# Optimization experiments

Hardware: AMD Instinct MI355X
Metric: run time of the kernel (lower is better)

The kernel has to match this reference:

```python
import jax, jax.numpy as jnp
import numpy as np

N_NODES = 50000
N_EDGES = 600000
DIM_H = 128
LN_EPS = 1e-5


def setup_inputs() -> dict:
    key = jax.random.key(0)
    ks = jax.random.split(key, 8)
    s = 1.0 / np.sqrt(DIM_H)
    return {
        "nodes": jax.random.normal(ks[0], (N_NODES, DIM_H), jnp.float32),
        "W_msg": jax.random.normal(ks[1], (DIM_H, DIM_H), jnp.float32) * s,
        "b_msg": jnp.zeros((DIM_H,), jnp.float32),
        "w_ih": jax.random.normal(ks[2], (3 * DIM_H, DIM_H), jnp.float32) * s,
        "w_hh": jax.random.normal(ks[3], (3 * DIM_H, DIM_H), jnp.float32) * s,
        "b_ih": jnp.zeros((3 * DIM_H,), jnp.float32),
        "b_hh": jnp.zeros((3 * DIM_H,), jnp.float32),
        "ln_gamma": jnp.ones((DIM_H,), jnp.float32),
        "ln_beta": jnp.zeros((DIM_H,), jnp.float32),
        "edge_src": jax.random.randint(ks[4], (N_EDGES,), 0, N_NODES, jnp.int32),
        "edge_dst": jax.random.randint(ks[5], (N_EDGES,), 0, N_NODES, jnp.int32),
    }


def _layer_norm(x, gamma, beta):
    mu = jnp.mean(x, axis=-1, keepdims=True)
    var = jnp.mean(jnp.square(x - mu), axis=-1, keepdims=True)
    return gamma * (x - mu) * jax.lax.rsqrt(var + LN_EPS) + beta


def reference(nodes, W_msg, b_msg, w_ih, w_hh, b_ih, b_hh, ln_gamma, ln_beta,
              edge_src, edge_dst):
    n_nodes = nodes.shape[0]
    # send_and_recv: per-edge message from source node, sum-reduce at dest
    msg_e = nodes[edge_src] @ W_msg.T + b_msg            # [E, H] (irregular gather)
    messages = jax.ops.segment_sum(msg_e, edge_dst, num_segments=n_nodes)  # [N, H]
    # global connection: add mean node feature
    msg = messages + jnp.mean(nodes, axis=0)
    # single-step GRU (torch gate layout: r, z, n)
    gi = msg @ w_ih.T + b_ih                             # [N, 3H]
    gh = nodes @ w_hh.T + b_hh                           # [N, 3H]
    i_r, i_z, i_n = jnp.split(gi, 3, axis=-1)
    h_r, h_z, h_n = jnp.split(gh, 3, axis=-1)
    r = jax.nn.sigmoid(i_r + h_r)
    z = jax.nn.sigmoid(i_z + h_z)
    n = jnp.tanh(i_n + r * h_n)
    h_next = (1.0 - z) * n + z * nodes
    # LayerNorm then post-GRU spatial residual with messages
    out = _layer_norm(h_next, ln_gamma, ln_beta)
    out = out + messages
    return out
```

## Files before the change

### kernel.cpp

```cpp
#include <hip/hip_runtime.h>
#include <hip/hip_bf16.h>

#define N_NODES 50000
#define N_EDGES 600000
#define DIM_H   128
#define NPAD    50048
#define NB_SCAN 196

typedef __attribute__((ext_vector_type(8))) short bf16x8;
typedef __attribute__((ext_vector_type(4))) float f32x4;
typedef __attribute__((ext_vector_type(4))) short short4v;

__device__ __forceinline__ short f2bs(float f) {
    __hip_bfloat16 h = __float2bfloat16(f);
    return *reinterpret_cast<short*>(&h);
}
__device__ __forceinline__ float bs2f(short s) {
    unsigned u = ((unsigned)(unsigned short)s) << 16;
    return __builtin_bit_cast(float, u);
}
__device__ __forceinline__ float sigm(float x) { return 1.f / (1.f + __expf(-x)); }
__device__ __forceinline__ float tanh_f(float x) {
    return 2.f / (1.f + __expf(-2.f * x)) - 1.f;
}
__device__ __forceinline__ unsigned pk2(float a, float b) {
    return ((unsigned)(unsigned short)f2bs(b) << 16) | (unsigned)(unsigned short)f2bs(a);
}
__device__ __forceinline__ float unlo(unsigned u) { return bs2f((short)(u & 0xffffu)); }
__device__ __forceinline__ float unhi(unsigned u) { return bs2f((short)(u >> 16)); }

__device__ __forceinline__ void dma16(const void* g, const void* lds_uniform) {
    __builtin_amdgcn_global_load_lds(
        (const __attribute__((address_space(1))) void*)g,
        (__attribute__((address_space(3))) void*)(unsigned)(unsigned long long)lds_uniform,
        16, 0, 0);
}

__global__ __launch_bounds__(256) void prep_k(const float* __restrict__ wmsg,
                                              const float* __restrict__ wih,
                                              const float* __restrict__ whh,
                                              short* __restrict__ wmsgB,
                                              short* __restrict__ wihB,
                                              short* __restrict__ whhB,
                                              int* __restrict__ cnt,
                                              float* __restrict__ colsum,
                                              short* __restrict__ aggTail,
                                              short* __restrict__ nodesTail) {
    int i = blockIdx.x * 256 + threadIdx.x;
    if (i < 16384) wmsgB[i] = f2bs(wmsg[i]);
    if (i < 49152) { wihB[i] = f2bs(wih[i]); whhB[i] = f2bs(whh[i]); }
    if (i < N_NODES) cnt[i] = 0;
    if (i < 128) colsum[i] = 0.f;
    if (i < 1536) {
        short4v z = {0, 0, 0, 0};
        *(short4v*)(aggTail   + i * 4) = z;
        *(short4v*)(nodesTail + i * 4) = z;
    }
}

__global__ __launch_bounds__(256) void colsum_k(const float* __restrict__ nodes,
                                                float* __restrict__ colsum,
                                                short* __restrict__ nodesB) {
    __shared__ float red[8][128];
    const int tid = threadIdx.x;
    const int cg = tid & 31;
    const int rl = tid >> 5;
    float4 acc = {0.f, 0.f, 0.f, 0.f};
    for (int r = blockIdx.x * 8 + rl; r < N_NODES; r += gridDim.x * 8) {
        float4 v = *(const float4*)(nodes + (size_t)r * DIM_H + cg * 4);
        acc.x += v.x; acc.y += v.y; acc.z += v.z; acc.w += v.w;
        *(short4v*)(nodesB + (size_t)r * DIM_H + cg * 4) =
            (short4v){f2bs(v.x), f2bs(v.y), f2bs(v.z), f2bs(v.w)};
    }
    *(float4*)&red[rl][cg * 4] = acc;
    __syncthreads();
    if (tid < 128) {
        float s = 0.f;
#pragma unroll
        for (int i = 0; i < 8; ++i) s += red[i][tid];
        unsafeAtomicAdd(&colsum[tid], s);
    }
}

__global__ __launch_bounds__(256) void hist_k(const int* __restrict__ edst,
                                              int* __restrict__ cnt) {
    int e = blockIdx.x * 256 + threadIdx.x;
    if (e < N_EDGES) atomicAdd(&cnt[edst[e]], 1);
}

__global__ __launch_bounds__(256) void bsum_k(const int* __restrict__ cnt,
                                              int* __restrict__ bsum) {
    const int t = threadIdx.x;
    int i = blockIdx.x * 256 + t;
    int v = (i < N_NODES) ? cnt[i] : 0;
#pragma unroll
    for (int o = 32; o; o >>= 1) v += __shfl_xor(v, o, 64);
    __shared__ int w4[4];
    if ((t & 63) == 0) w4[t >> 6] = v;
    __syncthreads();
    if (t == 0) bsum[blockIdx.x] = w4[0] + w4[1] + w4[2] + w4[3];
}

__global__ __launch_bounds__(256) void scan2_k(const int* __restrict__ cnt,
                                               const int* __restrict__ bsum,
                                               int* __restrict__ rowptr,
                                               int* __restrict__ pos) {
    const int b = blockIdx.x, t = threadIdx.x;
    const int lane = t & 63, w = t >> 6;
    __shared__ int red[4];
    __shared__ int wsum[4];

    int ov = (t < b) ? bsum[t] : 0;
#pragma unroll
    for (int o = 32; o; o >>= 1) ov += __shfl_xor(ov, o, 64);
    if (lane == 0) red[w] = ov;
    __syncthreads();
    const int offset = red[0] + red[1] + red[2] + red[3];

    int i = b * 256 + t;
    int v = (i < N_NODES) ? cnt[i] : 0;
    int x = v;
#pragma unroll
    for (int o = 1; o < 64; o <<= 1) {
        int y = __shfl_up(x, o, 64);
        if (lane >= o) x += y;
    }
    if (lane == 63) wsum[w] = x;
    __syncthreads();
    int woff = 0;
#pragma unroll
    for (int j = 0; j < 4; ++j)
        if (j < w) woff += wsum[j];
    int excl = offset + woff + (x - v);
    if (i < N_NODES) { rowptr[i] = excl; pos[i] = excl; }
    if (i == N_NODES - 1) rowptr[N_NODES] = excl + v;
}

__global__ __launch_bounds__(256) void reorder_k(const int* __restrict__ esrc,
                                                 const int* __restrict__ edst,
                                                 int* __restrict__ pos,
                                                 int* __restrict__ ssrc) {
    int e = blockIdx.x * 256 + threadIdx.x;
    if (e < N_EDGES) {
        int p = atomicAdd(&pos[edst[e]], 1);
        ssrc[p] = esrc[e];
    }
}

__global__ __launch_bounds__(256) void aggregate_k(const short* __restrict__ nodesB,
                                                   const int* __restrict__ rowptr,
                                                   const int* __restrict__ ssrc,
                                                   short* __restrict__ aggB) {
    const int wid = threadIdx.x >> 6;
    const int lane = threadIdx.x & 63;
    const int n = blockIdx.x * 4 + wid;
    if (n >= N_NODES) return;
    const int s0 = rowptr[n], s1 = rowptr[n + 1];
    float2 acc = {0.f, 0.f};
    int e = s0;
    for (; e + 3 < s1; e += 4) {
        int sa = ssrc[e], sb = ssrc[e + 1], sc = ssrc[e + 2], sd = ssrc[e + 3];
        short2 va = ((const short2*)(nodesB + (size_t)sa * DIM_H))[lane];
        short2 vb = ((const short2*)(nodesB + (size_t)sb * DIM_H))[lane];
        short2 vc = ((const short2*)(nodesB + (size_t)sc * DIM_H))[lane];
        short2 vd = ((const short2*)(nodesB + (size_t)sd * DIM_H))[lane];
        acc.x += (bs2f(va.x) + bs2f(vb.x)) + (bs2f(vc.x) + bs2f(vd.x));
        acc.y += (bs2f(va.y) + bs2f(vb.y)) + (bs2f(vc.y) + bs2f(vd.y));
    }
    for (; e < s1; ++e) {
        int sa = ssrc[e];
        short2 va = ((const short2*)(nodesB + (size_t)sa * DIM_H))[lane];
        acc.x += bs2f(va.x);
        acc.y += bs2f(va.y);
    }
    short2 o; o.x = f2bs(acc.x); o.y = f2bs(acc.y);
    ((short2*)(aggB + (size_t)n * DIM_H))[lane] = o;
}

template <int ROWS>
__device__ __forceinline__ void stage_tileT(const short* __restrict__ src, int row0,
                                            short* lds, int w, int lane) {
    constexpr int ITERS = ROWS / 16;
#pragma unroll
    for (int it = 0; it < ITERS; ++it) {
        int c = w * ITERS + it;
        int s = c * 64 + lane;
        int r = s >> 4, q = s & 15;
        int g = q ^ (r & 15);
        dma16(src + (((size_t)(row0 + r)) << 7) + (g << 3), lds + (size_t)c * 512);
    }
}

__device__ __forceinline__ void wave_mm64(const short* __restrict__ A,
                                          const short* __restrict__ W,
                                          f32x4 (&acc)[2][4],
                                          int wm, int wn, int r16, int half) {
#pragma unroll
    for (int kt = 0; kt < 4; ++kt) {
        const int kg = kt * 4 + half;
        const int sq = (kg ^ r16) << 3;
        bf16x8 af[2], bfr[4];
#pragma unroll
        for (int t = 0; t < 2; ++t)
            af[t] = *(const bf16x8*)&A[(wm + t * 16 + r16) * 128 + sq];
#pragma unroll
        for (int t = 0; t < 4; ++t)
            bfr[t] = *(const bf16x8*)&W[(wn + t * 16 + r16) * 128 + sq];
#pragma unroll
        for (int i = 0; i < 2; ++i)
#pragma unroll
            for (int j = 0; j < 4; ++j)
                acc[i][j] = __builtin_amdgcn_mfma_f32_16x16x32_bf16(
                    af[i], bfr[j], acc[i][j], 0, 0, 0);
    }
}

#define ZACC()                                        \
    _Pragma("unroll") for (int zi = 0; zi < 2; ++zi)  \
    _Pragma("unroll") for (int zj = 0; zj < 4; ++zj)  \
        acc[zi][zj] = (f32x4){0.f, 0.f, 0.f, 0.f}

__global__ __launch_bounds__(256) void fused_k(const short* __restrict__ aggB,
                                               const short* __restrict__ nodesB,
                                               const short* __restrict__ wmsgB,
                                               const short* __restrict__ wihB,
                                               const short* __restrict__ whhB,
                                               const float* __restrict__ bmsg,
                                               const float* __restrict__ bih,
                                               const float* __restrict__ bhh,
                                               const int* __restrict__ deg,
                                               const float* __restrict__ colsum,
                                               const float* __restrict__ gamma,
                                               const float* __restrict__ beta,
                                               float* __restrict__ out) {
    __shared__ short Ms[64 * 128];
    __shared__ short Ns[64 * 128];
    __shared__ short Wb[128 * 128];
    __shared__ float redS[64][2];
    __shared__ float redQ[64][2];

    const int tid = threadIdx.x;
    const int lane = tid & 63, w = tid >> 6;
    const int m0 = blockIdx.x * 64;
    const int r16 = lane & 15, half = lane >> 4;
    const int wm = (w >> 1) * 32, wn = (w & 1) * 64;
    const float invN = 1.0f / N_NODES;

    stage_tileT<64>(aggB, m0, Ms, w, lane);
    stage_tileT<64>(nodesB, m0, Ns, w, lane);
    stage_tileT<128>(wmsgB, 0, Wb, w, lane);
    __syncthreads();

    f32x4 acc[2][4];

    ZACC();
    wave_mm64(Ms, Wb, acc, wm, wn, r16, half);
    __syncthreads();
    stage_tileT<128>(wihB, 0, Wb, w, lane);
    {
        float bm[4], cs[4];
#pragma unroll
        for (int j = 0; j < 4; ++j) {
            int c = wn + j * 16 + r16;
            bm[j] = bmsg[c];
            cs[j] = colsum[c] * invN;
        }
#pragma unroll
        for (int i = 0; i < 2; ++i)
#pragma unroll
            for (int rr = 0; rr < 4; ++rr) {
                int lr = wm + i * 16 + half * 4 + rr;
                int gm = m0 + lr;
                float dg = (gm < N_NODES) ? (float)deg[gm] : 0.f;
#pragma unroll
                for (int j = 0; j < 4; ++j) {
                    int c = wn + j * 16 + r16;
                    float v = acc[i][j][rr] + dg * bm[j] + cs[j];
                    int slot = (c >> 3) ^ (lr & 15);
                    Ms[lr * 128 + slot * 8 + (c & 7)] = f2bs(v);
                }
            }
    }
    __syncthreads();

    ZACC();
    wave_mm64(Ms, Wb, acc, wm, wn, r16, half);
    __syncthreads();
    stage_tileT<128>(whhB, 0, Wb, w, lane);
    __syncthreads();
    wave_mm64(Ns, Wb, acc, wm, wn, r16, half);
    __syncthreads();
    stage_tileT<128>(wihB, 256, Wb, w, lane);
    unsigned rp[2][4][2];
    {
        float b0[4];
#pragma unroll
        for (int j = 0; j < 4; ++j) {
            int c = wn + j * 16 + r16;
            b0[j] = bih[c] + bhh[c];
        }
#pragma unroll
        for (int i = 0; i < 2; ++i)
#pragma unroll
            for (int j = 0; j < 4; ++j) {
                rp[i][j][0] = pk2(sigm(acc[i][j][0] + b0[j]), sigm(acc[i][j][1] + b0[j]));
                rp[i][j][1] = pk2(sigm(acc[i][j][2] + b0[j]), sigm(acc[i][j][3] + b0[j]));
            }
    }
    __syncthreads();

    ZACC();
    wave_mm64(Ms, Wb, acc, wm, wn, r16, half);
    __syncthreads();
    stage_tileT<128>(whhB, 256, Wb, w, lane);
    unsigned inp[2][4][2];
    {
        float bi[4];
#pragma unroll
        for (int j = 0; j < 4; ++j) bi[j] = bih[256 + wn + j * 16 + r16];
#pragma unroll
        for (int i = 0; i < 2; ++i)
#pragma unroll
            for (int j = 0; j < 4; ++j) {
                inp[i][j][0] = pk2(acc[i][j][0] + bi[j], acc[i][j][1] + bi[j]);
                inp[i][j][1] = pk2(acc[i][j][2] + bi[j], acc[i][j][3] + bi[j]);
            }
    }
    __syncthreads();

    ZACC();
    wave_mm64(Ns, Wb, acc, wm, wn, r16, half);
    __syncthreads();
    stage_tileT<128>(wihB, 128, Wb, w, lane);
    unsigned np_[2][4][2];
    {
        float bh[4];
#pragma unroll
        for (int j = 0; j < 4; ++j) bh[j] = bhh[256 + wn + j * 16 + r16];
#pragma unroll
        for (int i = 0; i < 2; ++i)
#pragma unroll
            for (int j = 0; j < 4; ++j) {
                float n0 = tanh_f(unlo(inp[i][j][0]) + unlo(rp[i][j][0]) * (acc[i][j][0] + bh[j]));
                float n1 = tanh_f(unhi(inp[i][j][0]) + unhi(rp[i][j][0]) * (acc[i][j][1] + bh[j]));
                float n2 = tanh_f(unlo(inp[i][j][1]) + unlo(rp[i][j][1]) * (acc[i][j][2] + bh[j]));
                float n3 = tanh_f(unhi(inp[i][j][1]) + unhi(rp[i][j][1]) * (acc[i][j][3] + bh[j]));
                np_[i][j][0] = pk2(n0, n1);
                np_[i][j][1] = pk2(n2, n3);
            }
    }
    __syncthreads();

    ZACC();
    wave_mm64(Ms, Wb, acc, wm, wn, r16, half);
    __syncthreads();
    stage_tileT<128>(whhB, 128, Wb, w, lane);
    __syncthreads();
    wave_mm64(Ns, Wb, acc, wm, wn, r16, half);
    {
        float b1[4];
#pragma unroll
        for (int j = 0; j < 4; ++j) {
            int c = wn + j * 16 + r16;
            b1[j] = bih[128 + c] + bhh[128 + c];
        }
#pragma unroll
        for (int i = 0; i < 2; ++i)
#pragma unroll
            for (int j = 0; j < 4; ++j)
#pragma unroll
                for (int rr = 0; rr < 4; ++rr) {
                    int lr = wm + i * 16 + half * 4 + rr;
                    int c = wn + j * 16 + r16;
                    int slot = (c >> 3) ^ (lr & 15);
                    float h = bs2f(Ns[lr * 128 + slot * 8 + (c & 7)]);
                    float z = sigm(acc[i][j][rr] + b1[j]);
                    float nv = (rr & 1) ? unhi(np_[i][j][rr >> 1]) : unlo(np_[i][j][rr >> 1]);
                    acc[i][j][rr] = (1.f - z) * nv + z * h;
                }
    }

#pragma unroll
    for (int i = 0; i < 2; ++i)
#pragma unroll
        for (int rr = 0; rr < 4; ++rr) {
            float s = acc[i][0][rr] + acc[i][1][rr] + acc[i][2][rr] + acc[i][3][rr];
            float q = acc[i][0][rr] * acc[i][0][rr] + acc[i][1][rr] * acc[i][1][rr]
                    + acc[i][2][rr] * acc[i][2][rr] + acc[i][3][rr] * acc[i][3][rr];
#pragma unroll
            for (int o = 1; o < 16; o <<= 1) {
                s += __shfl_xor(s, o, 64);
                q += __shfl_xor(q, o, 64);
            }
            if (r16 == 0) {
                int lr = wm + i * 16 + half * 4 + rr;
                redS[lr][wn >> 6] = s;
                redQ[lr][wn >> 6] = q;
            }
        }
    __syncthreads();

    {
        float ga[4], be[4], cs[4];
#pragma unroll
        for (int j = 0; j < 4; ++j) {
            int c = wn + j * 16 + r16;
            ga[j] = gamma[c];
            be[j] = beta[c];
            cs[j] = colsum[c] * invN;
        }
#pragma unroll
        for (int i = 0; i < 2; ++i)
#pragma unroll
            for (int rr = 0; rr < 4; ++rr) {
                int lr = wm + i * 16 + half * 4 + rr;
                int gm = m0 + lr;
                float S = redS[lr][0] + redS[lr][1];
                float Q = redQ[lr][0] + redQ[lr][1];
                float mu = S * (1.0f / DIM_H);
                float var = Q * (1.0f / DIM_H) - mu * mu;
                float rstd = rsqrtf(var + 1e-5f);
                if (gm < N_NODES) {
#pragma unroll
                    for (int j = 0; j < 4; ++j) {
                        int c = wn + j * 16 + r16;
                        int slot = (c >> 3) ^ (lr & 15);
                        float resid = bs2f(Ms[lr * 128 + slot * 8 + (c & 7)]) - cs[j];
                        out[(size_t)gm * DIM_H + c] =
                            ga[j] * (acc[i][j][rr] - mu) * rstd + be[j] + resid;
                    }
                }
            }
    }
}

extern "C" void kernel_launch(void* const* d_in, const int* in_sizes, int n_in,
                              void* d_out, int out_size, void* d_ws, size_t ws_size,
                              hipStream_t stream) {
    const float* nodes = (const float*)d_in[0];
    const float* Wmsg  = (const float*)d_in[1];
    const float* bmsg  = (const float*)d_in[2];
    const float* wih   = (const float*)d_in[3];
    const float* whh   = (const float*)d_in[4];
    const float* bih   = (const float*)d_in[5];
    const float* bhh   = (const float*)d_in[6];
    const float* gamma = (const float*)d_in[7];
    const float* beta  = (const float*)d_in[8];
    const int* esrc = (const int*)d_in[9];
    const int* edst = (const int*)d_in[10];
    float* out = (float*)d_out;

    char* ws = (char*)d_ws;
    short* aggB   = (short*)ws;
    short* nodesB = (short*)(ws + 12812288);
    short* wmsgB  = (short*)(ws + 25624576);
    short* wihB   = (short*)(ws + 25657344);
    short* whhB   = (short*)(ws + 25755648);
    float* colsum = (float*)(ws + 25853952);
    int*   cnt    = (int*)(ws + 25854464);
    int*   rowptr = (int*)(ws + 26054464);
    int*   pos    = (int*)(ws + 26254480);
    int*   ssrc   = (int*)(ws + 26454480);
    int*   bsum   = (int*)(ws + 28854480);

    short* aggTail   = aggB   + (size_t)N_NODES * DIM_H;
    short* nodesTail = nodesB + (size_t)N_NODES * DIM_H;

    prep_k<<<NB_SCAN, 256, 0, stream>>>(Wmsg, wih, whh, wmsgB, wihB, whhB,
                                        cnt, colsum, aggTail, nodesTail);
    colsum_k<<<512, 256, 0, stream>>>(nodes, colsum, nodesB);

    const int EB = (N_EDGES + 255) / 256;
    hist_k<<<EB, 256, 0, stream>>>(edst, cnt);
    bsum_k<<<NB_SCAN, 256, 0, stream>>>(cnt, bsum);
    scan2_k<<<NB_SCAN, 256, 0, stream>>>(cnt, bsum, rowptr, pos);
    reorder_k<<<EB, 256, 0, stream>>>(esrc, edst, pos, ssrc);
    aggregate_k<<<(N_NODES + 3) / 4, 256, 0, stream>>>(nodesB, rowptr, ssrc, aggB);

    const int MB = (N_NODES + 63) / 64;
    fused_k<<<MB, 256, 0, stream>>>(aggB, nodesB, wmsgB, wihB, whhB,
                                    bmsg, bih, bhh, cnt, colsum, gamma, beta, out);
}
```

Before: 260.3 us.

## Read GEMM weight fragments directly from global memory instead of LDS staging

The fused GRU kernel now loads the weight B-fragments for each MFMA straight from global memory (L2-resident bf16 weights) rather than staging every 128x128 weight tile into shared memory. This removes the per-gate DMA staging and most block-wide barriers, and shrinks LDS use by 32KB. A launch-bounds occupancy hint of 3 blocks per CU is added. In exchange, each wave issues redundant uncoalesced 16-byte global loads for weights, relying on cache hits, and the higher occupancy target may limit registers.

```diff
diff --git a/kernel.cpp b/kernel.cpp
--- a/kernel.cpp
+++ b/kernel.cpp
@@ -191,10 +191,10 @@
     }
 }
 
-__device__ __forceinline__ void wave_mm64(const short* __restrict__ A,
-                                          const short* __restrict__ W,
-                                          f32x4 (&acc)[2][4],
-                                          int wm, int wn, int r16, int half) {
+__device__ __forceinline__ void wave_mm_gw(const short* __restrict__ A,
+                                           const short* __restrict__ Wg,
+                                           f32x4 (&acc)[2][4],
+                                           int wm, int wn, int r16, int half) {
 #pragma unroll
     for (int kt = 0; kt < 4; ++kt) {
         const int kg = kt * 4 + half;
@@ -205,7 +205,7 @@
             af[t] = *(const bf16x8*)&A[(wm + t * 16 + r16) * 128 + sq];
 #pragma unroll
         for (int t = 0; t < 4; ++t)
-            bfr[t] = *(const bf16x8*)&W[(wn + t * 16 + r16) * 128 + sq];
+            bfr[t] = *(const bf16x8*)&Wg[(size_t)(wn + t * 16 + r16) * 128 + kg * 8];
 #pragma unroll
         for (int i = 0; i < 2; ++i)
 #pragma unroll
@@ -220,22 +220,21 @@
     _Pragma("unroll") for (int zj = 0; zj < 4; ++zj)  \
         acc[zi][zj] = (f32x4){0.f, 0.f, 0.f, 0.f}
 
-__global__ __launch_bounds__(256) void fused_k(const short* __restrict__ aggB,
-                                               const short* __restrict__ nodesB,
-                                               const short* __restrict__ wmsgB,
-                                               const short* __restrict__ wihB,
-                                               const short* __restrict__ whhB,
-                                               const float* __restrict__ bmsg,
-                                               const float* __restrict__ bih,
-                                               const float* __restrict__ bhh,
-                                               const int* __restrict__ deg,
-                                               const float* __restrict__ colsum,
-                                               const float* __restrict__ gamma,
-                                               const float* __restrict__ beta,
-                                               float* __restrict__ out) {
+__global__ __launch_bounds__(256, 3) void fused_k(const short* __restrict__ aggB,
+                                                  const short* __restrict__ nodesB,
+                                                  const short* __restrict__ wmsgB,
+                                                  const short* __restrict__ wihB,
+                                                  const short* __restrict__ whhB,
+                                                  const float* __restrict__ bmsg,
+                                                  const float* __restrict__ bih,
+                                                  const float* __restrict__ bhh,
+                                                  const int* __restrict__ deg,
+                                                  const float* __restrict__ colsum,
+                                                  const float* __restrict__ gamma,
+                                                  const float* __restrict__ beta,
+                                                  float* __restrict__ out) {
     __shared__ short Ms[64 * 128];
     __shared__ short Ns[64 * 128];
-    __shared__ short Wb[128 * 128];
     __shared__ float redS[64][2];
     __shared__ float redQ[64][2];
 
@@ -248,15 +247,13 @@
 
     stage_tileT<64>(aggB, m0, Ms, w, lane);
     stage_tileT<64>(nodesB, m0, Ns, w, lane);
-    stage_tileT<128>(wmsgB, 0, Wb, w, lane);
     __syncthreads();
 
     f32x4 acc[2][4];
 
     ZACC();
-    wave_mm64(Ms, Wb, acc, wm, wn, r16, half);
-    __syncthreads();
-    stage_tileT<128>(wihB, 0, Wb, w, lane);
+    wave_mm_gw(Ms, wmsgB, acc, wm, wn, r16, half);
+    __syncthreads();
     {
         float bm[4], cs[4];
 #pragma unroll
@@ -284,13 +281,8 @@
     __syncthreads();
 
     ZACC();
-    wave_mm64(Ms, Wb, acc, wm, wn, r16, half);
-    __syncthreads();
-    stage_tileT<128>(whhB, 0, Wb, w, lane);
-    __syncthreads();
-    wave_mm64(Ns, Wb, acc, wm, wn, r16, half);
-    __syncthreads();
-    stage_tileT<128>(wihB, 256, Wb, w, lane);
+    wave_mm_gw(Ms, wihB, acc, wm, wn, r16, half);
+    wave_mm_gw(Ns, whhB, acc, wm, wn, r16, half);
     unsigned rp[2][4][2];
     {
         float b0[4];
@@ -307,12 +299,9 @@
                 rp[i][j][1] = pk2(sigm(acc[i][j][2] + b0[j]), sigm(acc[i][j][3] + b0[j]));
             }
     }
-    __syncthreads();
 
     ZACC();
-    wave_mm64(Ms, Wb, acc, wm, wn, r16, half);
-    __syncthreads();
-    stage_tileT<128>(whhB, 256, Wb, w, lane);
+    wave_mm_gw(Ms, wihB + 256 * 128, acc, wm, wn, r16, half);
     unsigned inp[2][4][2];
     {
         float bi[4];
@@ -326,12 +315,9 @@
                 inp[i][j][1] = pk2(acc[i][j][2] + bi[j], acc[i][j][3] + bi[j]);
             }
     }
-    __syncthreads();
 
     ZACC();
-    wave_mm64(Ns, Wb, acc, wm, wn, r16, half);
-    __syncthreads();
-    stage_tileT<128>(wihB, 128, Wb, w, lane);
+    wave_mm_gw(Ns, whhB + 256 * 128, acc, wm, wn, r16, half);
     unsigned np_[2][4][2];
     {
         float bh[4];
@@ -349,14 +335,10 @@
                 np_[i][j][1] = pk2(n2, n3);
             }
     }
-    __syncthreads();
 
     ZACC();
-    wave_mm64(Ms, Wb, acc, wm, wn, r16, half);
-    __syncthreads();
-    stage_tileT<128>(whhB, 128, Wb, w, lane);
-    __syncthreads();
-    wave_mm64(Ns, Wb, acc, wm, wn, r16, half);
+    wave_mm_gw(Ms, wihB + 128 * 128, acc, wm, wn, r16, half);
+    wave_mm_gw(Ns, whhB + 128 * 128, acc, wm, wn, r16, half);
     {
         float b1[4];
 #pragma unroll
```

New measurement: 316.1 us. 21.5% more time.
